# Optimization experiments

Measured on AMD Instinct MI355X. Metric: run time of the kernel, lower is better.

The kernel has to match this reference:

```python
import jax, jax.numpy as jnp
import numpy as np

LMAX = 2
C1 = 64; C2 = 64; COUT = 64
B = 4096
SUM_RDIM = sum(3**L for L in range(LMAX + 1))   # 13
FEAT1 = C1 * SUM_RDIM                            # 832
FEAT2 = C2 * SUM_RDIM


def _enumerate_paths(Lmax):
    paths = []
    for L1 in range(Lmax + 1):
        for L2 in range(Lmax + 1):
            for k in range(min(L1, L2) + 1):
                Lout = L1 + L2 - 2 * k
                if 0 <= Lout <= Lmax:
                    paths.append((L1, L2, Lout, k, False))
            if L1 >= 1 and L2 >= 1:
                for k in range(min(L1 - 1, L2 - 1) + 1):
                    Lout = L1 + L2 - 2 * k - 1
                    if 0 <= Lout <= Lmax:
                        paths.append((L1, L2, Lout, k, True))
    return paths

PATHS = _enumerate_paths(LMAX)   # 15 paths for Lmax=2


def _path_eq(L1, L2, k, use_eps):
    # Fused equation: W[c,a,b] contracted together with the delta/eps path einsum.
    letters = list('defghijklmnopqrstuvwxyz')  # a,b,c reserved for channels
    i_idx = letters[:L1]
    j_idx = letters[L1:L1 + L2]
    for r in range(k):  # delta: contract last k indices of A with last k of B
        j_idx[L2 - k + r] = i_idx[L1 - k + r]
    i_free = i_idx[:L1 - k]
    j_free = j_idx[:L2 - k]
    eps_sub = None
    if use_eps:  # consume last free index of each side via eps_{p i j}
        p = letters[L1 + L2]
        eps_sub = p + i_free[-1] + j_free[-1]
        i_free, j_free = i_free[:-1], j_free[:-1]
        out = i_free + j_free + [p]
    else:
        out = i_free + j_free
    terms = ['cab', '...a' + ''.join(i_idx), '...b' + ''.join(j_idx)]
    if eps_sub is not None:
        terms.append(eps_sub)
    return ','.join(terms) + '->...c' + ''.join(out)


def _epsilon():
    e = np.zeros((3, 3, 3), dtype=np.float32)
    e[0, 1, 2] = e[1, 2, 0] = e[2, 0, 1] = 1.0
    e[2, 1, 0] = e[1, 0, 2] = e[0, 2, 1] = -1.0
    return jnp.asarray(e)


def _split_by_rank(x, C, Lmax):
    batch = x.shape[:-1]
    out, idx = {}, 0
    for L in range(Lmax + 1):
        d = C * 3**L
        blk = x[..., idx:idx + d]
        idx += d
        out[L] = blk.reshape(*batch, C) if L == 0 else blk.reshape(*batch, C, *((3,) * L))
    return out


def setup_inputs() -> dict:
    key = jax.random.key(0)
    k1, k2, k3 = jax.random.split(key, 3)
    x1 = jax.random.normal(k1, (B, FEAT1), dtype=jnp.float32)
    x2 = jax.random.normal(k2, (B, FEAT2), dtype=jnp.float32)
    weight = jax.random.normal(k3, (len(PATHS) * COUT * C1 * C2,), dtype=jnp.float32) * 0.02
    return {"x1": x1, "x2": x2, "weight": weight}


def reference(x1, x2, weight):
    A = _split_by_rank(x1, C1, LMAX)
    Bt = _split_by_rank(x2, C2, LMAX)
    eps = _epsilon().astype(x1.dtype)
    batch = x1.shape[:-1]
    blocks = {L: jnp.zeros((*batch, COUT) + (3,) * L, dtype=x1.dtype) for L in range(LMAX + 1)}
    wsz = COUT * C1 * C2
    for n, (L1, L2, Lout, k, use_eps) in enumerate(PATHS):
        Wp = weight[n * wsz:(n + 1) * wsz].reshape(COUT, C1, C2)
        eq = _path_eq(L1, L2, k, use_eps)
        ops = (Wp, A[L1], Bt[L2]) + ((eps,) if use_eps else ())
        blocks[Lout] = blocks[Lout] + jnp.einsum(eq, *ops, optimize='optimal')
    parts = [blocks[L].reshape(*batch, COUT * 3**L) for L in range(LMAX + 1)]
    return jnp.concatenate(parts, axis=-1)
```

## Files before the change

### kernel.cpp

```cpp
#include <hip/hip_runtime.h>
#include <cstdint>
#include <cstddef>


#define FEAT 832
#define ZT 64

typedef _Float16 half8 __attribute__((ext_vector_type(8)));
typedef float floatx16 __attribute__((ext_vector_type(16)));

struct Chunk {
  int wbase;
  int o1[3];
  int o2[3];
  float sg[3];
  int d1, d2, nt;
};

__global__ void swz_w_kernel(const float* __restrict__ w, _Float16* __restrict__ o) {
  const int i = blockIdx.x * 256 + threadIdx.x;
  const int lane = i & 63;
  const int pkc  = i >> 6;
  const int cgrp = pkc & 1;
  const int ksg  = (pkc >> 1) & 255;
  const int p    = pkc >> 9;
  const int c  = cgrp * 32 + (lane & 31);
  const int k0 = ksg * 16 + (lane >> 5) * 8;
  const float* src = w + (size_t)p * 262144 + (size_t)c * 4096 + k0;
  const float4 v0 = *(const float4*)(src);
  const float4 v1 = *(const float4*)(src + 4);
  half8 h = { (_Float16)v0.x, (_Float16)v0.y, (_Float16)v0.z, (_Float16)v0.w,
              (_Float16)v1.x, (_Float16)v1.y, (_Float16)v1.z, (_Float16)v1.w };
  *(half8*)(o + (size_t)i * 8) = h;
}

__global__ __launch_bounds__(256) void gather_kernel(
    float* __restrict__ out, const float* __restrict__ part, int np)
{
  __shared__ float T[64][65];
  const int zb = blockIdx.x * 64;
  const int fb = blockIdx.y * 64;
  const int tid = threadIdx.x;
  const int fl = tid >> 6;
  const int zl = tid & 63;
  #pragma unroll
  for (int i = 0; i < 16; ++i) {
    const int f = fb + fl + i * 4;
    int s, c;
    if (f < 64)       { s = 0;              c = f; }
    else if (f < 256) { const int g = f - 64;  c = g / 3; s = 1 + g % 3; }
    else              { const int g = f - 256; c = g / 9; s = 4 + g % 9; }
    const size_t base = (size_t)s * 262144 + (size_t)c * 4096 + zb + zl;
    float v = 0.0f;
    for (int q = 0; q < np; ++q)
      v += part[(size_t)q * 3407872 + base];
    T[fl + i * 4][zl] = v;
  }
  __syncthreads();
  const int zr = tid >> 6;
  const int fc = tid & 63;
  #pragma unroll
  for (int i = 0; i < 16; ++i) {
    const int z = zr + i * 4;
    float* o = out + (size_t)(zb + z) * FEAT + fb + fc;
    *o += T[fc][z];
  }
}

__device__ __forceinline__ half8 splat8(_Float16 h) {
  return half8{h, h, h, h, h, h, h, h};
}

template<int NT>
__device__ __forceinline__ void run_chunk(
    const Chunk C, const int zbase, const int zl, const int hf,
    const int lane, const int tid,
    const float* __restrict__ x1, const float* __restrict__ x2,
    const _Float16* __restrict__ Wh,
    _Float16* __restrict__ XS2, _Float16* __restrict__ XS1,
    floatx16& acc0, floatx16& acc1)
{
  __syncthreads();

  #pragma unroll
  for (int t = 0; t < NT; ++t) {
    const size_t base2 = (size_t)zbase * FEAT + C.o2[t];
    for (int e = tid; e < 4096; e += 128) {
      const int zz = e >> 6, b = e & 63;
      XS2[(t * 64 + zz) * 72 + b] =
          (_Float16)x2[base2 + (size_t)zz * FEAT + b * C.d2];
    }
  }
  #pragma unroll
  for (int t = 0; t < NT; ++t) {
    const float sgf = C.sg[t];
    const int o1 = C.o1[t];
    for (int e = tid; e < 4096; e += 128) {
      const int a = e & 63, zz = e >> 6;
      XS1[(t * 64 + a) * 66 + zz] =
          (_Float16)(x1[(size_t)(zbase + zz) * FEAT + o1 + a * C.d1] * sgf);
    }
  }
  __syncthreads();

  half8 x2r[NT][4];
  #pragma unroll
  for (int t = 0; t < NT; ++t) {
    #pragma unroll
    for (int ks = 0; ks < 4; ++ks)
      x2r[t][ks] = *(const half8*)&XS2[(t * 64 + zl) * 72 + ks * 16 + hf * 8];
  }

  const _Float16* __restrict__ Wq = Wh + C.wbase + lane * 8;
  const _Float16* __restrict__ Xq = XS1 + zl;

  half8 afE[2][4], afO[2][4];
  #pragma unroll
  for (int ks = 0; ks < 4; ++ks) {
    afE[0][ks] = *(const half8*)(Wq + ks * 1024);
    afE[1][ks] = *(const half8*)(Wq + ks * 1024 + 512);
    afO[0][ks] = *(const half8*)(Wq + 4096 + ks * 1024);
    afO[1][ks] = *(const half8*)(Wq + 4096 + ks * 1024 + 512);
  }
  _Float16 sc[NT], scn[NT];
  #pragma unroll
  for (int t = 0; t < NT; ++t) {
    sc[t]  = Xq[(t * 64 + 0) * 66];
    scn[t] = Xq[(t * 64 + 1) * 66];
  }

  #pragma unroll 1
  for (int a = 0; a < 64; a += 2) {
    {
      half8 sv[NT];
      #pragma unroll
      for (int t = 0; t < NT; ++t) sv[t] = splat8(sc[t]);
      if (a + 2 < 64) {
        #pragma unroll
        for (int t = 0; t < NT; ++t) sc[t] = Xq[(t * 64 + a + 2) * 66];
      }
      #pragma unroll
      for (int ks = 0; ks < 4; ++ks) {
        half8 tb = sv[0] * x2r[0][ks];
        if (NT > 1) tb += sv[1] * x2r[1][ks];
        if (NT > 2) tb += sv[2] * x2r[2][ks];
        acc0 = __builtin_amdgcn_mfma_f32_32x32x16_f16(afE[0][ks], tb, acc0, 0, 0, 0);
        acc1 = __builtin_amdgcn_mfma_f32_32x32x16_f16(afE[1][ks], tb, acc1, 0, 0, 0);
      }
      if (a + 2 < 64) {
        const _Float16* wn = Wq + (a + 2) * 4096;
        #pragma unroll
        for (int ks = 0; ks < 4; ++ks) {
          afE[0][ks] = *(const half8*)(wn + ks * 1024);
          afE[1][ks] = *(const half8*)(wn + ks * 1024 + 512);
        }
      }
    }
    {
      half8 sv[NT];
      #pragma unroll
      for (int t = 0; t < NT; ++t) sv[t] = splat8(scn[t]);
      if (a + 3 < 64) {
        #pragma unroll
        for (int t = 0; t < NT; ++t) scn[t] = Xq[(t * 64 + a + 3) * 66];
      }
      #pragma unroll
      for (int ks = 0; ks < 4; ++ks) {
        half8 tb = sv[0] * x2r[0][ks];
        if (NT > 1) tb += sv[1] * x2r[1][ks];
        if (NT > 2) tb += sv[2] * x2r[2][ks];
        acc0 = __builtin_amdgcn_mfma_f32_32x32x16_f16(afO[0][ks], tb, acc0, 0, 0, 0);
        acc1 = __builtin_amdgcn_mfma_f32_32x32x16_f16(afO[1][ks], tb, acc1, 0, 0, 0);
      }
      if (a + 3 < 64) {
        const _Float16* wn = Wq + (a + 3) * 4096;
        #pragma unroll
        for (int ks = 0; ks < 4; ++ks) {
          afO[0][ks] = *(const half8*)(wn + ks * 1024);
          afO[1][ks] = *(const half8*)(wn + ks * 1024 + 512);
        }
      }
    }
  }
}

__global__ __launch_bounds__(128, 2) void tp_kernel(
    const float* __restrict__ x1, const float* __restrict__ x2,
    const _Float16* __restrict__ Wh, float* __restrict__ out,
    float* __restrict__ part)
{
  __shared__ __align__(16) _Float16 XS2[3 * 64 * 72];
  __shared__ __align__(16) _Float16 XS1[3 * 64 * 66];
  __shared__ Chunk chs[7];
  __shared__ int nch_s;

  const int tid  = threadIdx.x;
  const int slot = blockIdx.y;
  const int q    = blockIdx.z;
  const int nsplit = gridDim.z;
  const int zbase = blockIdx.x * ZT;
  const int zgrp = tid >> 6;
  const int lane = tid & 63;
  const int ln31 = lane & 31;
  const int hf   = lane >> 5;
  const int zl   = zgrp * 32 + ln31;

  int offO, dO, mO;
  if (slot == 0)      { offO = 0;   dO = 1; mO = 0; }
  else if (slot < 4)  { offO = 64;  dO = 3; mO = slot - 1; }
  else                { offO = 256; dO = 9; mO = slot - 4; }

  if (tid == 0) {
    int n = 0;
    auto add = [&](int p, int L1, int L2,
                   int i0, int i1, int i2, int j0, int j1, int j2,
                   float s0, float s1, float s2, int nt) {
      const int offs[3] = {0, 64, 256};
      const int ds[3]   = {1, 3, 9};
      Chunk c;
      c.wbase = p * 262144;
      c.o1[0] = offs[L1] + i0; c.o1[1] = offs[L1] + i1; c.o1[2] = offs[L1] + i2;
      c.o2[0] = offs[L2] + j0; c.o2[1] = offs[L2] + j1; c.o2[2] = offs[L2] + j2;
      c.sg[0] = s0; c.sg[1] = s1; c.sg[2] = s2;
      c.d1 = ds[L1]; c.d2 = ds[L2]; c.nt = nt;
      chs[n++] = c;
    };
    if (slot == 0) {
      add(0, 0,0, 0,0,0, 0,0,0, 1,0,0, 1);
      add(5, 1,1, 0,1,2, 0,1,2, 1,1,1, 3);
      add(13,2,2, 0,1,2, 0,1,2, 1,1,1, 3);
      add(13,2,2, 3,4,5, 3,4,5, 1,1,1, 3);
      add(13,2,2, 6,7,8, 6,7,8, 1,1,1, 3);
    } else if (slot < 4) {
      const int m = slot - 1, p1 = (m+1)%3, p2 = (m+2)%3;
      add(1, 0,1, 0,0,0, m,0,0, 1,0,0, 1);
      add(3, 1,0, m,0,0, 0,0,0, 1,0,0, 1);
      add(6, 1,1, p1,p2,0, p2,p1,0, 1,-1,0, 2);
      add(7, 1,2, 0,1,2, 3*m,3*m+1,3*m+2, 1,1,1, 3);
      add(10,2,1, 3*m,3*m+1,3*m+2, 0,1,2, 1,1,1, 3);
      add(14,2,2, 3*p1,3*p1+1,3*p1+2, 3*p2,3*p2+1,3*p2+2, 1,1,1, 3);
      add(14,2,2, 3*p2,3*p2+1,3*p2+2, 3*p1,3*p1+1,3*p1+2, -1,-1,-1, 3);
    } else {
      const int m = slot - 4, u = m/3, v = m%3, q1 = (v+1)%3, q2 = (v+2)%3;
      add(2, 0,2, 0,0,0, m,0,0, 1,0,0, 1);
      add(4, 1,1, u,0,0, v,0,0, 1,0,0, 1);
      add(8, 1,2, q1,q2,0, 3*u+q2,3*u+q1,0, 1,-1,0, 2);
      add(9, 2,0, m,0,0, 0,0,0, 1,0,0, 1);
      add(11,2,1, 3*u+q1,3*u+q2,0, q2,q1,0, 1,-1,0, 2);
      add(12,2,2, 3*u,3*u+1,3*u+2, 3*v,3*v+1,3*v+2, 1,1,1, 3);
    }
    nch_s = n;
  }
  __syncthreads();
  const int nch = nch_s;

  floatx16 acc0, acc1;
  #pragma unroll
  for (int r = 0; r < 16; ++r) { acc0[r] = 0.0f; acc1[r] = 0.0f; }

  for (int ci = q; ci < nch; ci += nsplit) {
    const Chunk C = chs[ci];
    if (C.nt == 1)      run_chunk<1>(C, zbase, zl, hf, lane, tid, x1, x2, Wh, XS2, XS1, acc0, acc1);
    else if (C.nt == 2) run_chunk<2>(C, zbase, zl, hf, lane, tid, x1, x2, Wh, XS2, XS1, acc0, acc1);
    else                run_chunk<3>(C, zbase, zl, hf, lane, tid, x1, x2, Wh, XS2, XS1, acc0, acc1);
  }

  if (q == 0) {
    float* __restrict__ op = out + (size_t)(zbase + zl) * FEAT + offO + mO;
    #pragma unroll
    for (int r = 0; r < 16; ++r) {
      const int cr = (r & 3) + 8 * (r >> 2) + 4 * hf;
      op[(size_t)cr * dO]        = acc0[r];
      op[(size_t)(cr + 32) * dO] = acc1[r];
    }
  } else {
    float* __restrict__ op = part + (size_t)(q - 1) * 3407872
                                  + (size_t)slot * 262144 + (zbase + zl);
    #pragma unroll
    for (int r = 0; r < 16; ++r) {
      const int cr = (r & 3) + 8 * (r >> 2) + 4 * hf;
      op[(size_t)cr * 4096]        = acc0[r];
      op[(size_t)(cr + 32) * 4096] = acc1[r];
    }
  }
}

extern "C" void kernel_launch(void* const* d_in, const int* in_sizes, int n_in,
                              void* d_out, int out_size, void* d_ws, size_t ws_size,
                              hipStream_t stream) {
  const float* x1 = (const float*)d_in[0];
  const float* x2 = (const float*)d_in[1];
  const float* w  = (const float*)d_in[2];
  float* out = (float*)d_out;
  _Float16* Wh = (_Float16*)d_ws;
  float* part = (float*)((char*)d_ws + 7864320);

  const size_t plane_bytes = 3407872ull * 4ull;
  int np = (ws_size > 7864320) ? (int)((ws_size - 7864320) / plane_bytes) : 1;
  if (np > 3) np = 3;
  if (np < 1) np = 1;
  const int nsplit = np + 1;

  const int nchunks = 15 * 64 * 4096 / 8;
  hipLaunchKernelGGL(swz_w_kernel, dim3(nchunks / 256), dim3(256), 0, stream, w, Wh);

  dim3 grid(64, 13, nsplit);
  hipLaunchKernelGGL(tp_kernel, grid, dim3(128), 0, stream, x1, x2, Wh, out, part);

  dim3 ggrid(64, 13);
  hipLaunchKernelGGL(gather_kernel, ggrid, dim3(256), 0, stream, out, part, np);
}
```

Before: 377.1 us.

## Load x2 fragments directly from global into registers, drop XS2 LDS staging

The x2 operand is now read straight from global memory into each lane's half8 register fragments instead of being staged through a shared-memory XS2 tile. Three-term chunks read contiguous float triples (f3) for both x1 and x2. This removes the XS2 LDS buffer and its write/read traffic, which lowers LDS usage and may allow more occupancy. The cost is strided, poorly coalesced per-lane global loads of x2, and the f3 loads assume the three sub-chunks have contiguous offsets with stride 1.

```diff
diff --git a/kernel.cpp b/kernel.cpp
--- a/kernel.cpp
+++ b/kernel.cpp
@@ -8,6 +8,8 @@
 
 typedef _Float16 half8 __attribute__((ext_vector_type(8)));
 typedef float floatx16 __attribute__((ext_vector_type(16)));
+
+struct __attribute__((aligned(4))) f3 { float x, y, z; };
 
 struct Chunk {
   int wbase;
@@ -76,40 +78,65 @@
     const Chunk C, const int zbase, const int zl, const int hf,
     const int lane, const int tid,
     const float* __restrict__ x1, const float* __restrict__ x2,
-    const _Float16* __restrict__ Wh,
-    _Float16* __restrict__ XS2, _Float16* __restrict__ XS1,
+    const _Float16* __restrict__ Wh, _Float16* __restrict__ XS1,
     floatx16& acc0, floatx16& acc1)
 {
   __syncthreads();
 
-  #pragma unroll
-  for (int t = 0; t < NT; ++t) {
-    const size_t base2 = (size_t)zbase * FEAT + C.o2[t];
-    for (int e = tid; e < 4096; e += 128) {
-      const int zz = e >> 6, b = e & 63;
-      XS2[(t * 64 + zz) * 72 + b] =
-          (_Float16)x2[base2 + (size_t)zz * FEAT + b * C.d2];
-    }
-  }
-  #pragma unroll
-  for (int t = 0; t < NT; ++t) {
-    const float sgf = C.sg[t];
-    const int o1 = C.o1[t];
+  half8 x2r[NT][4];
+  {
+    const float* __restrict__ x2z = x2 + (size_t)(zbase + zl) * FEAT;
+    if (NT == 3) {
+      const float* __restrict__ p = x2z + C.o2[0];
+      #pragma unroll
+      for (int ks = 0; ks < 4; ++ks) {
+        const int b0 = ks * 16 + hf * 8;
+        #pragma unroll
+        for (int j = 0; j < 8; ++j) {
+          const f3 v = *(const f3*)(p + (b0 + j) * C.d2);
+          x2r[0][ks][j] = (_Float16)v.x;
+          x2r[1][ks][j] = (_Float16)v.y;
+          x2r[2][ks][j] = (_Float16)v.z;
+        }
+      }
+    } else {
+      #pragma unroll
+      for (int t = 0; t < NT; ++t) {
+        const float* __restrict__ p = x2z + C.o2[t];
+        #pragma unroll
+        for (int ks = 0; ks < 4; ++ks) {
+          const int b0 = ks * 16 + hf * 8;
+          #pragma unroll
+          for (int j = 0; j < 8; ++j)
+            x2r[t][ks][j] = (_Float16)p[(b0 + j) * C.d2];
+        }
+      }
+    }
+  }
+
+  if (NT == 3) {
+    const float s0 = C.sg[0], s1 = C.sg[1], s2 = C.sg[2];
+    const int o1 = C.o1[0];
     for (int e = tid; e < 4096; e += 128) {
       const int a = e & 63, zz = e >> 6;
-      XS1[(t * 64 + a) * 66 + zz] =
-          (_Float16)(x1[(size_t)(zbase + zz) * FEAT + o1 + a * C.d1] * sgf);
+      const f3 v = *(const f3*)(x1 + (size_t)(zbase + zz) * FEAT + o1 + a * C.d1);
+      XS1[(0 * 64 + a) * 66 + zz] = (_Float16)(v.x * s0);
+      XS1[(1 * 64 + a) * 66 + zz] = (_Float16)(v.y * s1);
+      XS1[(2 * 64 + a) * 66 + zz] = (_Float16)(v.z * s2);
+    }
+  } else {
+    #pragma unroll
+    for (int t = 0; t < NT; ++t) {
+      const float sgf = C.sg[t];
+      const int o1 = C.o1[t];
+      for (int e = tid; e < 4096; e += 128) {
+        const int a = e & 63, zz = e >> 6;
+        XS1[(t * 64 + a) * 66 + zz] =
+            (_Float16)(x1[(size_t)(zbase + zz) * FEAT + o1 + a * C.d1] * sgf);
+      }
     }
   }
   __syncthreads();
-
-  half8 x2r[NT][4];
-  #pragma unroll
-  for (int t = 0; t < NT; ++t) {
-    #pragma unroll
-    for (int ks = 0; ks < 4; ++ks)
-      x2r[t][ks] = *(const half8*)&XS2[(t * 64 + zl) * 72 + ks * 16 + hf * 8];
-  }
 
   const _Float16* __restrict__ Wq = Wh + C.wbase + lane * 8;
   const _Float16* __restrict__ Xq = XS1 + zl;
@@ -189,7 +216,6 @@
     const _Float16* __restrict__ Wh, float* __restrict__ out,
     float* __restrict__ part)
 {
-  __shared__ __align__(16) _Float16 XS2[3 * 64 * 72];
   __shared__ __align__(16) _Float16 XS1[3 * 64 * 66];
   __shared__ Chunk chs[7];
   __shared__ int nch_s;
@@ -260,9 +286,9 @@
 
   for (int ci = q; ci < nch; ci += nsplit) {
     const Chunk C = chs[ci];
-    if (C.nt == 1)      run_chunk<1>(C, zbase, zl, hf, lane, tid, x1, x2, Wh, XS2, XS1, acc0, acc1);
-    else if (C.nt == 2) run_chunk<2>(C, zbase, zl, hf, lane, tid, x1, x2, Wh, XS2, XS1, acc0, acc1);
-    else                run_chunk<3>(C, zbase, zl, hf, lane, tid, x1, x2, Wh, XS2, XS1, acc0, acc1);
+    if (C.nt == 1)      run_chunk<1>(C, zbase, zl, hf, lane, tid, x1, x2, Wh, XS1, acc0, acc1);
+    else if (C.nt == 2) run_chunk<2>(C, zbase, zl, hf, lane, tid, x1, x2, Wh, XS1, acc0, acc1);
+    else                run_chunk<3>(C, zbase, zl, hf, lane, tid, x1, x2, Wh, XS1, acc0, acc1);
   }
 
   if (q == 0) {
```

Measured after the change: 377.4 us. No clear change (+0.1%).
